# Optimization experiments

Measured on AMD Instinct MI355X. Metric: run time of the kernel, lower is better.

Reference implementation:

```python
import jax, jax.numpy as jnp
import numpy as np

B, N, H = 2, 512, 256


def setup_inputs() -> dict:
    key = jax.random.key(0)
    ks = jax.random.split(key, 12)
    s = 1.0 / np.sqrt(H)
    s2 = 1.0 / np.sqrt(2 * H)
    return {
        "step_sequence": jax.random.normal(ks[0], (B, N, H), dtype=jnp.float32),
        "step_mask": jnp.ones((B, N), dtype=jnp.float32),
        # graph_conv: two Linear(H,H) layers (each followed by ReLU)
        "W_gc1": jax.random.uniform(ks[1], (H, H), minval=-s, maxval=s),
        "b_gc1": jax.random.uniform(ks[2], (H,), minval=-s, maxval=s),
        "W_gc2": jax.random.uniform(ks[3], (H, H), minval=-s, maxval=s),
        "b_gc2": jax.random.uniform(ks[4], (H,), minval=-s, maxval=s),
        # edge_predictor: Linear(2H,H) -> ReLU -> Linear(H,1) -> Sigmoid
        "W_ep1": jax.random.uniform(ks[5], (H, 2 * H), minval=-s2, maxval=s2),
        "b_ep1": jax.random.uniform(ks[6], (H,), minval=-s2, maxval=s2),
        "w_ep2": jax.random.uniform(ks[7], (H,), minval=-s, maxval=s),
        "b_ep2": jax.random.uniform(ks[8], (), minval=-s, maxval=s),
    }


def reference(step_sequence, step_mask, W_gc1, b_gc1, W_gc2, b_gc2,
              W_ep1, b_ep1, w_ep2, b_ep2):
    # graph_conv: (Linear+ReLU) -> ReLU (idempotent) -> (Linear+ReLU)
    h = jax.nn.relu(step_sequence @ W_gc1.T + b_gc1)          # [B,N,H]
    f = jax.nn.relu(h @ W_gc2.T + b_gc2)                       # [B,N,H]
    # edge_predictor on concat(f_i, f_j): split first linear into halves
    Wa, Wb = W_ep1[:, :H], W_ep1[:, H:]
    a = jnp.einsum('bnh,kh->bnk', f, Wa)                       # [B,N,H]
    c = jnp.einsum('bnh,kh->bnk', f, Wb)                       # [B,N,H]
    e = jax.nn.relu(a[:, :, None, :] + c[:, None, :, :] + b_ep1)  # [B,N,N,H]
    scores = jax.nn.sigmoid(jnp.einsum('bijh,h->bij', e, w_ep2) + b_ep2)
    # strictly-lower-triangular causal mask (also zeros the diagonal / i==j)
    mask = jnp.tril(jnp.ones((N, N), dtype=scores.dtype), k=-1)
    return scores * mask
```

## Files before the change

### kernel.cpp

```cpp
#include <hip/hip_runtime.h>
#include <math.h>

#define NSEQ 512
#define MROWS 1024

typedef __attribute__((ext_vector_type(8))) short short8;
typedef __attribute__((ext_vector_type(4))) short short4v;
typedef __attribute__((ext_vector_type(4))) float f32x4;
typedef __attribute__((ext_vector_type(8))) _Float16 half8v;
typedef __attribute__((ext_vector_type(2))) _Float16 half2v;

static __device__ __forceinline__ short f2bf(float f) {
    unsigned u = __float_as_uint(f);
    unsigned r = (u + 0x7fffu + ((u >> 16) & 1u)) >> 16;
    return (short)r;
}
static __device__ __forceinline__ short h2s(_Float16 h) {
    short s; __builtin_memcpy(&s, &h, 2); return s;
}

__global__ __launch_bounds__(256) void gemm_mfma(
    const float* __restrict__ A, const float* __restrict__ W, int ldw, int colOff,
    const float* __restrict__ bias, int biasN,
    float* __restrict__ C, int ldc, int relu, int ntx)
{
    __shared__ short As[32 * 256];
    __shared__ short Ws[32 * 256];

    const int t  = threadIdx.x;
    const int m0 = ((int)blockIdx.x / ntx) * 32;
    const int n0 = ((int)blockIdx.x % ntx) * 32;

    {
        const float* src = A + (size_t)m0 * 256;
        #pragma unroll
        for (int i = 0; i < 8; ++i) {
            const int fidx = (t + i * 256) * 4;
            float4 v = *(const float4*)(src + fidx);
            const int row = fidx >> 8, col = fidx & 255;
            const int sidx = row * 256 + (col ^ ((row & 7) << 3));
            short4v p; p.x = f2bf(v.x); p.y = f2bf(v.y); p.z = f2bf(v.z); p.w = f2bf(v.w);
            *(short4v*)&As[sidx] = p;
        }
    }
    {
        const int wr = t >> 3;
        const int gn = n0 + wr;
        const float* src = W + (size_t)(gn & 255) * ldw + (size_t)(gn >> 8) * colOff;
        const int cb = (t & 7) * 32;
        #pragma unroll
        for (int g = 0; g < 8; ++g) {
            const int col = cb + g * 4;
            float4 v = *(const float4*)(src + col);
            const int sidx = wr * 256 + (col ^ ((wr & 7) << 3));
            short4v p; p.x = f2bf(v.x); p.y = f2bf(v.y); p.z = f2bf(v.z); p.w = f2bf(v.w);
            *(short4v*)&Ws[sidx] = p;
        }
    }
    __syncthreads();

    const int wid = t >> 6, l = t & 63;
    const int fr = l & 15, fq = l >> 4;
    const int mb = (wid >> 1) * 16, nb = (wid & 1) * 16;
    const int arow = mb + fr, brow = nb + fr;

    f32x4 acc = {0.f, 0.f, 0.f, 0.f};
    #pragma unroll
    for (int kk = 0; kk < 8; ++kk) {
        const int col8 = kk * 32 + fq * 8;
        short8 af = *(const short8*)&As[arow * 256 + (col8 ^ ((arow & 7) << 3))];
        short8 bf = *(const short8*)&Ws[brow * 256 + (col8 ^ ((brow & 7) << 3))];
        acc = __builtin_amdgcn_mfma_f32_16x16x32_bf16(af, bf, acc, 0, 0, 0);
    }

    const int gcol = n0 + nb + fr;
    float bv = 0.f;
    if (bias && gcol < biasN) bv = bias[gcol];
    #pragma unroll
    for (int q = 0; q < 4; ++q) {
        const int grow = m0 + mb + fq * 4 + q;
        float v = acc[q] + bv;
        if (relu) v = fmaxf(v, 0.f);
        C[(size_t)grow * ldc + gcol] = v;
    }
}

__global__ __launch_bounds__(256) void gemm_mfma_ac(
    const float* __restrict__ A, const float* __restrict__ W,
    const float* __restrict__ bep,
    short* __restrict__ Ab, short* __restrict__ Cb)
{
    __shared__ short As[32 * 256];
    __shared__ short Ws[32 * 256];

    const int t  = threadIdx.x;
    const int m0 = ((int)blockIdx.x / 16) * 32;
    const int n0 = ((int)blockIdx.x % 16) * 32;

    {
        const float* src = A + (size_t)m0 * 256;
        #pragma unroll
        for (int i = 0; i < 8; ++i) {
            const int fidx = (t + i * 256) * 4;
            float4 v = *(const float4*)(src + fidx);
            const int row = fidx >> 8, col = fidx & 255;
            const int sidx = row * 256 + (col ^ ((row & 7) << 3));
            short4v p; p.x = f2bf(v.x); p.y = f2bf(v.y); p.z = f2bf(v.z); p.w = f2bf(v.w);
            *(short4v*)&As[sidx] = p;
        }
    }
    {
        const int wr = t >> 3;
        const int gn = n0 + wr;
        const float* src = W + (size_t)(gn & 255) * 512 + (size_t)(gn >> 8) * 256;
        const int cb = (t & 7) * 32;
        #pragma unroll
        for (int g = 0; g < 8; ++g) {
            const int col = cb + g * 4;
            float4 v = *(const float4*)(src + col);
            const int sidx = wr * 256 + (col ^ ((wr & 7) << 3));
            short4v p; p.x = f2bf(v.x); p.y = f2bf(v.y); p.z = f2bf(v.z); p.w = f2bf(v.w);
            *(short4v*)&Ws[sidx] = p;
        }
    }
    __syncthreads();

    const int wid = t >> 6, l = t & 63;
    const int fr = l & 15, fq = l >> 4;
    const int mb = (wid >> 1) * 16, nb = (wid & 1) * 16;
    const int arow = mb + fr, brow = nb + fr;

    f32x4 acc = {0.f, 0.f, 0.f, 0.f};
    #pragma unroll
    for (int kk = 0; kk < 8; ++kk) {
        const int col8 = kk * 32 + fq * 8;
        short8 af = *(const short8*)&As[arow * 256 + (col8 ^ ((arow & 7) << 3))];
        short8 bf = *(const short8*)&Ws[brow * 256 + (col8 ^ ((brow & 7) << 3))];
        acc = __builtin_amdgcn_mfma_f32_16x16x32_bf16(af, bf, acc, 0, 0, 0);
    }

    const int gcol = n0 + nb + fr;
    const float bv = (gcol < 256) ? bep[gcol] : 0.f;
    #pragma unroll
    for (int q = 0; q < 4; ++q) {
        const int grow = m0 + mb + fq * 4 + q;
        const float v = acc[q] + bv;
        if (gcol < 256) Ab[(size_t)grow * 256 + gcol]         = h2s((_Float16)v);
        else            Cb[(size_t)grow * 256 + (gcol - 256)] = h2s((_Float16)v);
    }
}

__device__ __forceinline__ float dot8(half8v x, half8v w, float s) {
    s = __builtin_amdgcn_fdot2(__builtin_shufflevector(x, x, 0, 1),
                               __builtin_shufflevector(w, w, 0, 1), s, false);
    s = __builtin_amdgcn_fdot2(__builtin_shufflevector(x, x, 2, 3),
                               __builtin_shufflevector(w, w, 2, 3), s, false);
    s = __builtin_amdgcn_fdot2(__builtin_shufflevector(x, x, 4, 5),
                               __builtin_shufflevector(w, w, 4, 5), s, false);
    s = __builtin_amdgcn_fdot2(__builtin_shufflevector(x, x, 6, 7),
                               __builtin_shufflevector(w, w, 6, 7), s, false);
    return s;
}

__global__ __launch_bounds__(256) void pair_k(
    const short* __restrict__ Ab, const short* __restrict__ Cb,
    const float* __restrict__ wv, const float* __restrict__ b2p,
    float* __restrict__ out)
{
    __shared__ short lds[4][2 * 16 * 256 + 256];

    const int t    = threadIdx.x;
    const int wave = t >> 6, l = t & 63;
    const int tile = (int)blockIdx.x * 4 + wave;
    const int b    = tile >> 10;
    const int r_   = tile & 1023;
    const int it   = r_ >> 5, jt = r_ & 31;
    const int i0   = it * 16, j0 = jt * 16;
    float* outb = out + (size_t)b * NSEQ * NSEQ;

    if (jt > it) {
        const int rr = l >> 2, cc = (l & 3) * 4;
        *(float4*)(outb + (size_t)(i0 + rr) * NSEQ + j0 + cc) =
            make_float4(0.f, 0.f, 0.f, 0.f);
        return;
    }

    short* A_l = &lds[wave][0];
    short* C_l = &lds[wave][16 * 256];
    short* W_l = &lds[wave][2 * 16 * 256];

    {
        const int lrow = l >> 5;
        const int cc   = l & 31;
        const size_t abase = (size_t)(b * NSEQ + i0) * 256;
        const size_t cbase = (size_t)(b * NSEQ + j0) * 256;
        short8 areg[8], creg[8];
        #pragma unroll
        for (int q = 0; q < 8; ++q) {
            const int row = q * 2 + lrow;
            areg[q] = *(const short8*)(Ab + abase + row * 256 + cc * 8);
            creg[q] = *(const short8*)(Cb + cbase + row * 256 + cc * 8);
        }
        float4 w4 = *(const float4*)(wv + l * 4);
        #pragma unroll
        for (int q = 0; q < 8; ++q) {
            const int row = q * 2 + lrow;
            const int sw  = (cc ^ (row & 7)) * 8;
            *(short8*)&A_l[row * 256 + sw] = areg[q];
            *(short8*)&C_l[row * 256 + sw] = creg[q];
        }
        short4v wp;
        wp.x = h2s((_Float16)w4.x); wp.y = h2s((_Float16)w4.y);
        wp.z = h2s((_Float16)w4.z); wp.w = h2s((_Float16)w4.w);
        *(short4v*)&W_l[l * 4] = wp;
    }

    const int ti = l >> 3, tj = l & 7;
    float s00 = 0.f, s01 = 0.f, s10 = 0.f, s11 = 0.f;
    const half8v z8 = (half8v)(_Float16)0.f;

    #pragma unroll 8
    for (int cc = 0; cc < 32; ++cc) {
        half8v a0 = *(const half8v*)&A_l[ ti      * 256 + ((cc ^ ( ti      & 7)) * 8)];
        half8v a1 = *(const half8v*)&A_l[(ti + 8) * 256 + ((cc ^ ((ti + 8) & 7)) * 8)];
        half8v c0 = *(const half8v*)&C_l[ tj      * 256 + ((cc ^ ( tj      & 7)) * 8)];
        half8v c1 = *(const half8v*)&C_l[(tj + 8) * 256 + ((cc ^ ((tj + 8) & 7)) * 8)];
        half8v w8 = *(const half8v*)&W_l[cc * 8];
        half8v x;
        x = __builtin_elementwise_max(a0 + c0, z8); s00 = dot8(x, w8, s00);
        x = __builtin_elementwise_max(a0 + c1, z8); s01 = dot8(x, w8, s01);
        x = __builtin_elementwise_max(a1 + c0, z8); s10 = dot8(x, w8, s10);
        x = __builtin_elementwise_max(a1 + c1, z8); s11 = dot8(x, w8, s11);
    }

    const float bias2 = *b2p;
    const int i1 = i0 + ti, i2 = i0 + ti + 8;
    const int j1 = j0 + tj, j2 = j0 + tj + 8;
    const float r00 = 1.f / (1.f + expf(-(s00 + bias2)));
    const float r01 = 1.f / (1.f + expf(-(s01 + bias2)));
    const float r10 = 1.f / (1.f + expf(-(s10 + bias2)));
    const float r11 = 1.f / (1.f + expf(-(s11 + bias2)));
    outb[(size_t)i1 * NSEQ + j1] = (j1 < i1) ? r00 : 0.f;
    outb[(size_t)i1 * NSEQ + j2] = (j2 < i1) ? r01 : 0.f;
    outb[(size_t)i2 * NSEQ + j1] = (j1 < i2) ? r10 : 0.f;
    outb[(size_t)i2 * NSEQ + j2] = (j2 < i2) ? r11 : 0.f;
}

extern "C" void kernel_launch(void* const* d_in, const int* in_sizes, int n_in,
                              void* d_out, int out_size, void* d_ws, size_t ws_size,
                              hipStream_t stream)
{
    (void)in_sizes; (void)n_in; (void)out_size; (void)ws_size;
    const float* X    = (const float*)d_in[0];
    const float* Wg1  = (const float*)d_in[2];
    const float* bg1  = (const float*)d_in[3];
    const float* Wg2  = (const float*)d_in[4];
    const float* bg2  = (const float*)d_in[5];
    const float* Wep1 = (const float*)d_in[6];
    const float* bep1 = (const float*)d_in[7];
    const float* wep2 = (const float*)d_in[8];
    const float* bep2 = (const float*)d_in[9];
    float* out = (float*)d_out;

    float* hbuf = (float*)d_ws;
    float* fbuf = hbuf + MROWS * 256;
    short* Ab   = (short*)(fbuf + MROWS * 256);
    short* Cb   = Ab + MROWS * 256;

    const dim3 bb(256);
    hipLaunchKernelGGL(gemm_mfma, dim3(256), bb, 0, stream,
                       X, Wg1, 256, 0, bg1, 256, hbuf, 256, 1, 8);
    hipLaunchKernelGGL(gemm_mfma, dim3(256), bb, 0, stream,
                       hbuf, Wg2, 256, 0, bg2, 256, fbuf, 256, 1, 8);
    hipLaunchKernelGGL(gemm_mfma_ac, dim3(512), bb, 0, stream,
                       fbuf, Wep1, bep1, Ab, Cb);
    hipLaunchKernelGGL(pair_k, dim3(512), bb, 0, stream,
                       Ab, Cb, wep2, bep2, out);
}
```

Measured before the change: 31.30 us.

## Fuse the three MLP GEMMs into one row-blocked kernel with double-buffered weights

Replaces the three separate GEMM launches (gc1, gc2, edge projection) with one kernel in which each block owns 16 rows and keeps the intermediate activations in shared memory as bf16. Weight K-slices are streamed through double-buffered LDS with register prefetch. This removes two kernel launches and the fp32 round trips of h and f through global memory. In exchange only 64 blocks run, and each must stream all weight matrices, so parallelism is lower and weights are re-read per block.

Result: faster. 29.25 us (-6.6%).

```diff
diff --git a/kernel.cpp b/kernel.cpp
--- a/kernel.cpp
+++ b/kernel.cpp
@@ -8,7 +8,6 @@
 typedef __attribute__((ext_vector_type(4))) short short4v;
 typedef __attribute__((ext_vector_type(4))) float f32x4;
 typedef __attribute__((ext_vector_type(8))) _Float16 half8v;
-typedef __attribute__((ext_vector_type(2))) _Float16 half2v;
 
 static __device__ __forceinline__ short f2bf(float f) {
     unsigned u = __float_as_uint(f);
@@ -18,136 +17,131 @@
 static __device__ __forceinline__ short h2s(_Float16 h) {
     short s; __builtin_memcpy(&s, &h, 2); return s;
 }
-
-__global__ __launch_bounds__(256) void gemm_mfma(
-    const float* __restrict__ A, const float* __restrict__ W, int ldw, int colOff,
-    const float* __restrict__ bias, int biasN,
-    float* __restrict__ C, int ldc, int relu, int ntx)
-{
-    __shared__ short As[32 * 256];
-    __shared__ short Ws[32 * 256];
+static __device__ __forceinline__ short8 pack8(float4 a, float4 b) {
+    short8 r;
+    r[0] = f2bf(a.x); r[1] = f2bf(a.y); r[2] = f2bf(a.z); r[3] = f2bf(a.w);
+    r[4] = f2bf(b.x); r[5] = f2bf(b.y); r[6] = f2bf(b.z); r[7] = f2bf(b.w);
+    return r;
+}
+static __device__ __forceinline__ const float* wrow(
+    const float* __restrict__ W, int n, int ldw, int colOff) {
+    return W + (size_t)(n & 255) * ldw + (size_t)(n >> 8) * colOff;
+}
+
+template<int NOUT>
+__device__ __forceinline__ void w_load(float4* ra, float4* rb,
+    const float* __restrict__ W, int ldw, int colOff, int s, int t)
+{
+    #pragma unroll
+    for (int p = 0; p < NOUT / 128; ++p) {
+        const int n = p * 128 + (t >> 2), c = t & 3;
+        const float* src = wrow(W, n, ldw, colOff) + s * 32 + c * 8;
+        ra[p] = *(const float4*)src;
+        rb[p] = *(const float4*)(src + 4);
+    }
+}
+template<int NOUT>
+__device__ __forceinline__ void w_store(short* __restrict__ wb,
+    const float4* ra, const float4* rb, int t)
+{
+    #pragma unroll
+    for (int p = 0; p < NOUT / 128; ++p) {
+        const int n = p * 128 + (t >> 2), c = t & 3;
+        *(short8*)&wb[n * 32 + ((c ^ (n & 3)) * 8)] = pack8(ra[p], rb[p]);
+    }
+}
+
+template<int NOUT, int MODE>
+__device__ __forceinline__ void phase(short* wb0, short* wb1,
+    const short* __restrict__ actIn, short* __restrict__ actOut,
+    const float* __restrict__ W, int ldw, int colOff,
+    const float* __restrict__ bias,
+    short* __restrict__ Ab, short* __restrict__ Cb, int r0, int t)
+{
+    constexpr int NT = NOUT / 128;
+    {
+        float4 ra[NT], rb[NT];
+        w_load<NOUT>(ra, rb, W, ldw, colOff, 0, t);
+        w_store<NOUT>(wb0, ra, rb, t);
+    }
+    float4 ra[NT], rb[NT];
+    w_load<NOUT>(ra, rb, W, ldw, colOff, 1, t);
+    __syncthreads();
+
+    const int w = t >> 6, l = t & 63;
+    const int fr = l & 15, fq = l >> 4;
+    f32x4 acc[NT];
+    #pragma unroll
+    for (int i = 0; i < NT; ++i) acc[i] = (f32x4){0.f, 0.f, 0.f, 0.f};
+
+    #pragma unroll
+    for (int s = 0; s < 8; ++s) {
+        short* cur = (s & 1) ? wb1 : wb0;
+        short* nxt = (s & 1) ? wb0 : wb1;
+        if (s < 7) {
+            w_store<NOUT>(nxt, ra, rb, t);
+            if (s < 6) w_load<NOUT>(ra, rb, W, ldw, colOff, s + 2, t);
+        }
+        const short8 af = *(const short8*)
+            &actIn[fr * 256 + ((s * 32 + fq * 8) ^ ((fr & 7) << 3))];
+        #pragma unroll
+        for (int nt = 0; nt < NT; ++nt) {
+            const int n = w * (NT * 16) + nt * 16 + fr;
+            const short8 bf = *(const short8*)&cur[n * 32 + ((fq ^ (n & 3)) * 8)];
+            acc[nt] = __builtin_amdgcn_mfma_f32_16x16x32_bf16(af, bf, acc[nt], 0, 0, 0);
+        }
+        __syncthreads();
+    }
+
+    #pragma unroll
+    for (int nt = 0; nt < NT; ++nt) {
+        const int col = w * (NT * 16) + nt * 16 + fr;
+        if constexpr (MODE == 0) {
+            const float bv = bias[col];
+            #pragma unroll
+            for (int q = 0; q < 4; ++q) {
+                const int row = fq * 4 + q;
+                actOut[row * 256 + (col ^ ((row & 7) << 3))] =
+                    f2bf(fmaxf(acc[nt][q] + bv, 0.f));
+            }
+        } else {
+            const float bv = (col < 256) ? bias[col] : 0.f;
+            #pragma unroll
+            for (int q = 0; q < 4; ++q) {
+                const int grow = r0 + fq * 4 + q;
+                const float v = acc[nt][q] + bv;
+                if (col < 256) Ab[(size_t)grow * 256 + col]         = h2s((_Float16)v);
+                else           Cb[(size_t)grow * 256 + (col - 256)] = h2s((_Float16)v);
+            }
+        }
+    }
+}
+
+__global__ __launch_bounds__(512, 2) void chain_k(
+    const float* __restrict__ X,
+    const float* __restrict__ W1, const float* __restrict__ b1,
+    const float* __restrict__ W2, const float* __restrict__ b2,
+    const float* __restrict__ Wep, const float* __restrict__ bep,
+    short* __restrict__ Ab, short* __restrict__ Cb)
+{
+    __shared__ short wb[2][16384];
+    __shared__ short act[2][4096];
 
     const int t  = threadIdx.x;
-    const int m0 = ((int)blockIdx.x / ntx) * 32;
-    const int n0 = ((int)blockIdx.x % ntx) * 32;
+    const int r0 = (int)blockIdx.x * 16;
 
     {
-        const float* src = A + (size_t)m0 * 256;
-        #pragma unroll
-        for (int i = 0; i < 8; ++i) {
-            const int fidx = (t + i * 256) * 4;
-            float4 v = *(const float4*)(src + fidx);
-            const int row = fidx >> 8, col = fidx & 255;
-            const int sidx = row * 256 + (col ^ ((row & 7) << 3));
-            short4v p; p.x = f2bf(v.x); p.y = f2bf(v.y); p.z = f2bf(v.z); p.w = f2bf(v.w);
-            *(short4v*)&As[sidx] = p;
-        }
-    }
-    {
-        const int wr = t >> 3;
-        const int gn = n0 + wr;
-        const float* src = W + (size_t)(gn & 255) * ldw + (size_t)(gn >> 8) * colOff;
-        const int cb = (t & 7) * 32;
-        #pragma unroll
-        for (int g = 0; g < 8; ++g) {
-            const int col = cb + g * 4;
-            float4 v = *(const float4*)(src + col);
-            const int sidx = wr * 256 + (col ^ ((wr & 7) << 3));
-            short4v p; p.x = f2bf(v.x); p.y = f2bf(v.y); p.z = f2bf(v.z); p.w = f2bf(v.w);
-            *(short4v*)&Ws[sidx] = p;
-        }
-    }
-    __syncthreads();
-
-    const int wid = t >> 6, l = t & 63;
-    const int fr = l & 15, fq = l >> 4;
-    const int mb = (wid >> 1) * 16, nb = (wid & 1) * 16;
-    const int arow = mb + fr, brow = nb + fr;
-
-    f32x4 acc = {0.f, 0.f, 0.f, 0.f};
-    #pragma unroll
-    for (int kk = 0; kk < 8; ++kk) {
-        const int col8 = kk * 32 + fq * 8;
-        short8 af = *(const short8*)&As[arow * 256 + (col8 ^ ((arow & 7) << 3))];
-        short8 bf = *(const short8*)&Ws[brow * 256 + (col8 ^ ((brow & 7) << 3))];
-        acc = __builtin_amdgcn_mfma_f32_16x16x32_bf16(af, bf, acc, 0, 0, 0);
-    }
-
-    const int gcol = n0 + nb + fr;
-    float bv = 0.f;
-    if (bias && gcol < biasN) bv = bias[gcol];
-    #pragma unroll
-    for (int q = 0; q < 4; ++q) {
-        const int grow = m0 + mb + fq * 4 + q;
-        float v = acc[q] + bv;
-        if (relu) v = fmaxf(v, 0.f);
-        C[(size_t)grow * ldc + gcol] = v;
-    }
-}
-
-__global__ __launch_bounds__(256) void gemm_mfma_ac(
-    const float* __restrict__ A, const float* __restrict__ W,
-    const float* __restrict__ bep,
-    short* __restrict__ Ab, short* __restrict__ Cb)
-{
-    __shared__ short As[32 * 256];
-    __shared__ short Ws[32 * 256];
-
-    const int t  = threadIdx.x;
-    const int m0 = ((int)blockIdx.x / 16) * 32;
-    const int n0 = ((int)blockIdx.x % 16) * 32;
-
-    {
-        const float* src = A + (size_t)m0 * 256;
-        #pragma unroll
-        for (int i = 0; i < 8; ++i) {
-            const int fidx = (t + i * 256) * 4;
-            float4 v = *(const float4*)(src + fidx);
-            const int row = fidx >> 8, col = fidx & 255;
-            const int sidx = row * 256 + (col ^ ((row & 7) << 3));
-            short4v p; p.x = f2bf(v.x); p.y = f2bf(v.y); p.z = f2bf(v.z); p.w = f2bf(v.w);
-            *(short4v*)&As[sidx] = p;
-        }
-    }
-    {
-        const int wr = t >> 3;
-        const int gn = n0 + wr;
-        const float* src = W + (size_t)(gn & 255) * 512 + (size_t)(gn >> 8) * 256;
-        const int cb = (t & 7) * 32;
-        #pragma unroll
-        for (int g = 0; g < 8; ++g) {
-            const int col = cb + g * 4;
-            float4 v = *(const float4*)(src + col);
-            const int sidx = wr * 256 + (col ^ ((wr & 7) << 3));
-            short4v p; p.x = f2bf(v.x); p.y = f2bf(v.y); p.z = f2bf(v.z); p.w = f2bf(v.w);
-            *(short4v*)&Ws[sidx] = p;
-        }
-    }
-    __syncthreads();
-
-    const int wid = t >> 6, l = t & 63;
-    const int fr = l & 15, fq = l >> 4;
-    const int mb = (wid >> 1) * 16, nb = (wid & 1) * 16;
-    const int arow = mb + fr, brow = nb + fr;
-
-    f32x4 acc = {0.f, 0.f, 0.f, 0.f};
-    #pragma unroll
-    for (int kk = 0; kk < 8; ++kk) {
-        const int col8 = kk * 32 + fq * 8;
-        short8 af = *(const short8*)&As[arow * 256 + (col8 ^ ((arow & 7) << 3))];
-        short8 bf = *(const short8*)&Ws[brow * 256 + (col8 ^ ((brow & 7) << 3))];
-        acc = __builtin_amdgcn_mfma_f32_16x16x32_bf16(af, bf, acc, 0, 0, 0);
-    }
-
-    const int gcol = n0 + nb + fr;
-    const float bv = (gcol < 256) ? bep[gcol] : 0.f;
-    #pragma unroll
-    for (int q = 0; q < 4; ++q) {
-        const int grow = m0 + mb + fq * 4 + q;
-        const float v = acc[q] + bv;
-        if (gcol < 256) Ab[(size_t)grow * 256 + gcol]         = h2s((_Float16)v);
-        else            Cb[(size_t)grow * 256 + (gcol - 256)] = h2s((_Float16)v);
-    }
+        const int row = t >> 5, c = t & 31;
+        const float* src = X + (size_t)(r0 + row) * 256 + c * 8;
+        float4 v0 = *(const float4*)src, v1 = *(const float4*)(src + 4);
+        *(short8*)&act[0][row * 256 + ((c ^ (row & 7)) * 8)] = pack8(v0, v1);
+    }
+    phase<256, 0>(wb[0], wb[1], act[0], act[1], W1, 256, 0, b1,
+                  nullptr, nullptr, r0, t);
+    phase<256, 0>(wb[0], wb[1], act[1], act[0], W2, 256, 0, b2,
+                  nullptr, nullptr, r0, t);
+    phase<512, 1>(wb[0], wb[1], act[0], nullptr, Wep, 512, 256, bep,
+                  Ab, Cb, r0, t);
 }
 
 __device__ __forceinline__ float dot8(half8v x, half8v w, float s) {
@@ -262,18 +256,11 @@
     const float* bep2 = (const float*)d_in[9];
     float* out = (float*)d_out;
 
-    float* hbuf = (float*)d_ws;
-    float* fbuf = hbuf + MROWS * 256;
-    short* Ab   = (short*)(fbuf + MROWS * 256);
-    short* Cb   = Ab + MROWS * 256;
-
-    const dim3 bb(256);
-    hipLaunchKernelGGL(gemm_mfma, dim3(256), bb, 0, stream,
-                       X, Wg1, 256, 0, bg1, 256, hbuf, 256, 1, 8);
-    hipLaunchKernelGGL(gemm_mfma, dim3(256), bb, 0, stream,
-                       hbuf, Wg2, 256, 0, bg2, 256, fbuf, 256, 1, 8);
-    hipLaunchKernelGGL(gemm_mfma_ac, dim3(512), bb, 0, stream,
-                       fbuf, Wep1, bep1, Ab, Cb);
-    hipLaunchKernelGGL(pair_k, dim3(512), bb, 0, stream,
+    short* Ab = (short*)d_ws;
+    short* Cb = Ab + MROWS * 256;
+
+    hipLaunchKernelGGL(chain_k, dim3(64), dim3(512), 0, stream,
+                       X, Wg1, bg1, Wg2, bg2, Wep1, bep1, Ab, Cb);
+    hipLaunchKernelGGL(pair_k, dim3(512), dim3(256), 0, stream,
                        Ab, Cb, wep2, bep2, out);
 }
```
